# Performance work log

Measured on AMD Instinct MI355X. Metric: run time of the kernel, lower is better.

Reference implementation:

```python
import jax, jax.numpy as jnp
import numpy as np

B, T, D = 256, 512, 8      # batch, seq_len, Feature_number
H = 120                    # hidden_size
L = 4                      # layers=['s','s','s','s']
NH = D                     # num_heads = Feature_number
HD = H // NH               # head dim = 15
EPS = 1e-5


def setup_inputs() -> dict:
    key = jax.random.key(0)
    ks = jax.random.split(key, 16)
    rn = lambda k, shape, s=0.1: (jax.random.normal(k, shape, jnp.float32) * s)
    return {
        "x":   jax.random.normal(ks[0], (B, T, D), jnp.float32),
        # input->gate weights, stacked over layers
        "Wi":  rn(ks[1], (L, H, D)),
        "Wf":  rn(ks[2], (L, H, D)),
        "Wz":  rn(ks[3], (L, H, D)),
        "Wo":  rn(ks[4], (L, H, D)),
        # block-diagonal (multi-head) recurrent weights: [L, NH, HD, HD]
        "Ri":  rn(ks[5], (L, NH, HD, HD)),
        "Rf":  rn(ks[6], (L, NH, HD, HD)),
        "Rz":  rn(ks[7], (L, NH, HD, HD)),
        "Ro":  rn(ks[8], (L, NH, HD, HD)),
        "bi":  rn(ks[9],  (L, H), 0.02),
        "bf":  rn(ks[10], (L, H), 0.02),
        "bz":  rn(ks[11], (L, H), 0.02),
        "bo":  rn(ks[12], (L, H), 0.02),
        # per-block down-projection back to Feature_number (residual block)
        "Wp":  rn(ks[13], (L, D, H)),
        "bp":  jnp.zeros((L, D), jnp.float32),
        # BatchNorm1d(Feature_number) affine params
        "gamma": jnp.ones((D,), jnp.float32),
        "beta":  jnp.zeros((D,), jnp.float32),
        # fc5: Linear(Feature_number, 1)
        "Wfc": rn(ks[14], (1, D)),
        "bfc": jnp.zeros((1,), jnp.float32),
    }


def _slstm_layer(x, Wi, Wf, Wz, Wo, Ri, Rf, Rz, Ro, bi, bf, bz, bo, Wp, bp):
    """One sLSTM block: exp-gated recurrence with stabilizer, then down-proj + residual.
    x: [B, T, D] -> [B, T, D]."""
    Bn = x.shape[0]

    def rec(h, R):  # block-diagonal recurrent matmul: [B,H] x [NH,HD,HD] -> [B,H]
        return jnp.einsum("bnd,nde->bne", h.reshape(Bn, NH, HD), R).reshape(Bn, H)

    def step(carry, x_t):
        h, c, n, m = carry                       # each [B, H]
        it = x_t @ Wi.T + rec(h, Ri) + bi        # input gate pre-act
        ft = x_t @ Wf.T + rec(h, Rf) + bf        # forget gate pre-act (exp gating)
        z = jnp.tanh(x_t @ Wz.T + rec(h, Rz) + bz)
        o = jax.nn.sigmoid(x_t @ Wo.T + rec(h, Ro) + bo)
        m_new = jnp.maximum(ft + m, it)          # stabilizer state
        i_p = jnp.exp(it - m_new)
        f_p = jnp.exp(ft + m - m_new)
        c_new = f_p * c + i_p * z
        n_new = f_p * n + i_p                    # normalizer state
        h_new = o * (c_new / n_new)
        return (h_new, c_new, n_new, m_new), h_new

    z0 = jnp.zeros((Bn, H), x.dtype)
    (_, _, _, _), hs = jax.lax.scan(step, (z0, z0, z0, z0), jnp.swapaxes(x, 0, 1))
    y = jnp.einsum("tbh,dh->tbd", hs, Wp) + bp   # down-project to D
    return x + jnp.swapaxes(y, 0, 1)             # residual


def reference(x, Wi, Wf, Wz, Wo, Ri, Rf, Rz, Ro, bi, bf, bz, bo, Wp, bp,
              gamma, beta, Wfc, bfc):
    h = x
    for l in range(L):
        h = _slstm_layer(h, Wi[l], Wf[l], Wz[l], Wo[l], Ri[l], Rf[l], Rz[l], Ro[l],
                         bi[l], bf[l], bz[l], bo[l], Wp[l], bp[l])
    last = h[:, -1, :]                            # [B, D]
    # BatchNorm1d in training mode (batch stats, biased variance)
    mu = jnp.mean(last, axis=0)
    var = jnp.mean((last - mu) ** 2, axis=0)
    bn = (last - mu) / jnp.sqrt(var + EPS) * gamma + beta
    out = jax.nn.sigmoid(bn @ Wfc.T + bfc)        # [B, 1]
    return out[:, 0]                              # squeeze(1) -> [B]
```

## Files before the change

### kernel.cpp

```cpp
#include <hip/hip_runtime.h>
#include <math.h>

#define Bsz 256
#define T   512
#define Dd  8
#define Hh  120
#define Ll  4
#define NHn 8
#define HDd 15
#define HP  16
#define EPSf 1e-5f

__device__ __forceinline__ float fast_rcp(float x) {
#if __has_builtin(__builtin_amdgcn_rcpf)
    return __builtin_amdgcn_rcpf(x);
#else
    return 1.f / x;
#endif
}
__device__ __forceinline__ float tanh_fast(float x) {
    float e = __expf(2.f * x);
    return 1.f - 2.f * fast_rcp(e + 1.f);
}
__device__ __forceinline__ float sigm_fast(float x) {
    return fast_rcp(1.f + __expf(-x));
}

__global__ __launch_bounds__(512, 2) void slstm_kernel(
    const float* __restrict__ x,
    const float* __restrict__ Wi, const float* __restrict__ Wf,
    const float* __restrict__ Wz, const float* __restrict__ Wo,
    const float* __restrict__ Ri, const float* __restrict__ Rf,
    const float* __restrict__ Rz, const float* __restrict__ Ro,
    const float* __restrict__ bi, const float* __restrict__ bf,
    const float* __restrict__ bz, const float* __restrict__ bo,
    const float* __restrict__ Wp, const float* __restrict__ bp,
    float* __restrict__ last_out)
{
    __shared__ __align__(16) float xs[T * Dd];
    __shared__ __align__(16) float hb[Ll][2][NHn * HP];

    const int tid = threadIdx.x;
    const int b   = blockIdx.x;
    const int l   = tid >> 7;
    const int j   = tid & 127;

    {
        const float4* xg  = (const float4*)(x + (size_t)b * T * Dd);
        float4*       xs4 = (float4*)xs;
        xs4[tid]       = xg[tid];
        xs4[tid + 512] = xg[tid + 512];
        ((float*)hb)[tid]       = 0.f;
        ((float*)hb)[tid + 512] = 0.f;
    }

    const bool gl = (j < Hh);
    const int jj  = gl ? j : 0;
    const int n   = jj / HDd;
    const int e   = jj - n * HDd;
    float wI[Dd], wF[Dd], wZ[Dd], wO[Dd];
    float rI[HDd], rF[HDd], rZ[HDd], rO[HDd];
    {
        const int row = (l * Hh + jj) * Dd;
#pragma unroll
        for (int d = 0; d < Dd; ++d) {
            wI[d] = Wi[row + d]; wF[d] = Wf[row + d];
            wZ[d] = Wz[row + d]; wO[d] = Wo[row + d];
        }
        const int rb = ((l * NHn + n) * HDd) * HDd + e;
#pragma unroll
        for (int d = 0; d < HDd; ++d) {
            rI[d] = Ri[rb + d * HDd]; rF[d] = Rf[rb + d * HDd];
            rZ[d] = Rz[rb + d * HDd]; rO[d] = Ro[rb + d * HDd];
        }
    }
    float bI = bi[l * Hh + jj], bF = bf[l * Hh + jj];
    float bZ = bz[l * Hh + jj], bO = bo[l * Hh + jj];

    const int p  = (j >= 64) ? (j - 64) : j;
    const int d8 = p & 7, ch = p >> 3;
    float wp_r[16];
    {
        const int base = l * Dd * Hh + d8 * Hh + ch * HDd;
#pragma unroll
        for (int k = 0; k < HDd; ++k) wp_r[k] = Wp[base + k];
        wp_r[15] = 0.f;
    }
    float bp_r = bp[l * Dd + d8];

#pragma unroll
    for (int d = 0; d < Dd; ++d)
        asm volatile("" : "+v"(wI[d]), "+v"(wF[d]), "+v"(wZ[d]), "+v"(wO[d]));
#pragma unroll
    for (int d = 0; d < HDd; ++d)
        asm volatile("" : "+v"(rI[d]), "+v"(rF[d]), "+v"(rZ[d]), "+v"(rO[d]));
#pragma unroll
    for (int k = 0; k < 16; ++k)
        asm volatile("" : "+v"(wp_r[k]));
    asm volatile("" : "+v"(bI), "+v"(bF), "+v"(bZ), "+v"(bO));
    asm volatile("" : "+v"(bp_r));

    float cst = 0.f, nst = 0.f, mst = 0.f;

    __syncthreads();

    for (int tau = 0; tau < T + 2 * Ll - 1; ++tau) {
        const int t_g = tau - 2 * l;
        const int t_p = t_g - 1;

        if (gl && (t_g >= 0) && (t_g < T)) {
            const float4* xt4 = (const float4*)(xs + t_g * Dd);
            const float4 xa = xt4[0], xb2 = xt4[1];
            const float xv[Dd] = {xa.x, xa.y, xa.z, xa.w, xb2.x, xb2.y, xb2.z, xb2.w};
            float gi = bI, gf = bF, gz = bZ, go = bO;
#pragma unroll
            for (int d = 0; d < Dd; ++d) {
                gi = fmaf(xv[d], wI[d], gi);
                gf = fmaf(xv[d], wF[d], gf);
                gz = fmaf(xv[d], wZ[d], gz);
                go = fmaf(xv[d], wO[d], go);
            }
            const float4* h4 = (const float4*)(&hb[l][t_g & 1][n * HP]);
            const float4 h0 = h4[0], h1 = h4[1], h2 = h4[2], h3 = h4[3];
            const float hv[16] = {h0.x, h0.y, h0.z, h0.w, h1.x, h1.y, h1.z, h1.w,
                                  h2.x, h2.y, h2.z, h2.w, h3.x, h3.y, h3.z, h3.w};
#pragma unroll
            for (int d = 0; d < HDd; ++d) {
                gi = fmaf(hv[d], rI[d], gi);
                gf = fmaf(hv[d], rF[d], gf);
                gz = fmaf(hv[d], rZ[d], gz);
                go = fmaf(hv[d], rO[d], go);
            }
            const float z  = tanh_fast(gz);
            const float o  = sigm_fast(go);
            const float mn = fmaxf(gf + mst, gi);
            const float ip = __expf(gi - mn);
            const float fp = __expf(gf + mst - mn);
            cst = fmaf(fp, cst, ip * z);
            nst = fmaf(fp, nst, ip);
            mst = mn;
            const float hnew = o * cst * fast_rcp(nst);
            hb[l][(t_g & 1) ^ 1][n * HP + e] = hnew;
        }

        if ((j >= 64) && (t_p >= 0) && (t_p < T)) {
            const float4* h4 = (const float4*)(&hb[l][t_g & 1][ch * HP]);
            const float4 h0 = h4[0], h1 = h4[1], h2 = h4[2], h3 = h4[3];
            const float hv[16] = {h0.x, h0.y, h0.z, h0.w, h1.x, h1.y, h1.z, h1.w,
                                  h2.x, h2.y, h2.z, h2.w, h3.x, h3.y, h3.z, h3.w};
            float s = 0.f;
#pragma unroll
            for (int k = 0; k < 16; ++k) s = fmaf(hv[k], wp_r[k], s);
            s += __shfl_xor(s, 8);
            s += __shfl_xor(s, 16);
            s += __shfl_xor(s, 32);
            if (p < Dd) xs[t_p * Dd + p] += s + bp_r;
        }

        __syncthreads();
    }

    if (tid < Dd) last_out[b * Dd + tid] = xs[(T - 1) * Dd + tid];
}

__global__ __launch_bounds__(Bsz) void bn_fc_kernel(
    const float* __restrict__ last,
    const float* __restrict__ gamma, const float* __restrict__ beta,
    const float* __restrict__ Wfc,   const float* __restrict__ bfc,
    float* __restrict__ out)
{
    __shared__ float ls[Bsz][Dd];
    __shared__ float mu[Dd], rstdg[Dd], bet[Dd], wfc[Dd];
    const int tid = threadIdx.x;
#pragma unroll
    for (int d = 0; d < Dd; ++d) ls[tid][d] = last[tid * Dd + d];
    __syncthreads();
    if (tid < Dd) {
        float s = 0.f;
        for (int bb = 0; bb < Bsz; ++bb) s += ls[bb][tid];
        const float mean = s * (1.f / Bsz);
        float v = 0.f;
        for (int bb = 0; bb < Bsz; ++bb) {
            const float dd = ls[bb][tid] - mean;
            v += dd * dd;
        }
        v *= (1.f / Bsz);
        mu[tid]    = mean;
        rstdg[tid] = rsqrtf(v + EPSf) * gamma[tid];
        bet[tid]   = beta[tid];
        wfc[tid]   = Wfc[tid];
    }
    __syncthreads();
    float acc = bfc[0];
#pragma unroll
    for (int d = 0; d < Dd; ++d)
        acc += ((ls[tid][d] - mu[d]) * rstdg[d] + bet[d]) * wfc[d];
    out[tid] = sigm_fast(acc);
}

extern "C" void kernel_launch(void* const* d_in, const int* in_sizes, int n_in,
                              void* d_out, int out_size, void* d_ws, size_t ws_size,
                              hipStream_t stream) {
    const float* x    = (const float*)d_in[0];
    const float* Wi   = (const float*)d_in[1];
    const float* Wf   = (const float*)d_in[2];
    const float* Wz   = (const float*)d_in[3];
    const float* Wo   = (const float*)d_in[4];
    const float* Ri   = (const float*)d_in[5];
    const float* Rf   = (const float*)d_in[6];
    const float* Rz   = (const float*)d_in[7];
    const float* Ro   = (const float*)d_in[8];
    const float* bi   = (const float*)d_in[9];
    const float* bf   = (const float*)d_in[10];
    const float* bz   = (const float*)d_in[11];
    const float* bo   = (const float*)d_in[12];
    const float* Wp   = (const float*)d_in[13];
    const float* bp   = (const float*)d_in[14];
    const float* gamma= (const float*)d_in[15];
    const float* beta = (const float*)d_in[16];
    const float* Wfc  = (const float*)d_in[17];
    const float* bfc  = (const float*)d_in[18];

    float* last_ws = (float*)d_ws;
    float* out     = (float*)d_out;

    slstm_kernel<<<Bsz, 512, 0, stream>>>(x, Wi, Wf, Wz, Wo, Ri, Rf, Rz, Ro,
                                          bi, bf, bz, bo, Wp, bp, last_ws);
    bn_fc_kernel<<<1, Bsz, 0, stream>>>(last_ws, gamma, beta, Wfc, bfc, out);
}
```

Before: 453.1 us.

## Split each hidden unit's gates across two threads using packed FMAs

The block grows from 512 to 1024 threads. Each hidden unit is now handled by a thread pair: one lane computes the i/f pre-activations and the state update, the other computes z/o and passes them over with a lane shuffle. Each lane accumulates its two gates with 2-wide vector FMAs, which can map to packed FP32 instructions. The per-head stride in the shared hidden buffer is padded from 16 to 20 floats, likely to reduce LDS bank conflicts. This roughly halves the serial FMA chain per timestep, at the cost of extra shuffles, more resident threads and dropping the register-pinning asm.

After: 609.2 us. +34.4%, slower.

```diff
diff --git a/kernel.cpp b/kernel.cpp
--- a/kernel.cpp
+++ b/kernel.cpp
@@ -8,8 +8,10 @@
 #define Ll  4
 #define NHn 8
 #define HDd 15
-#define HP  16
+#define HP  20
 #define EPSf 1e-5f
+
+typedef float v2f __attribute__((ext_vector_type(2)));
 
 __device__ __forceinline__ float fast_rcp(float x) {
 #if __has_builtin(__builtin_amdgcn_rcpf)
@@ -25,8 +27,15 @@
 __device__ __forceinline__ float sigm_fast(float x) {
     return fast_rcp(1.f + __expf(-x));
 }
-
-__global__ __launch_bounds__(512, 2) void slstm_kernel(
+__device__ __forceinline__ v2f fma2(v2f a, v2f b, v2f c) {
+#if __has_builtin(__builtin_elementwise_fma)
+    return __builtin_elementwise_fma(a, b, c);
+#else
+    v2f r; r[0] = fmaf(a[0], b[0], c[0]); r[1] = fmaf(a[1], b[1], c[1]); return r;
+#endif
+}
+
+__global__ __launch_bounds__(1024, 4) void slstm_kernel(
     const float* __restrict__ x,
     const float* __restrict__ Wi, const float* __restrict__ Wf,
     const float* __restrict__ Wz, const float* __restrict__ Wo,
@@ -42,63 +51,49 @@
 
     const int tid = threadIdx.x;
     const int b   = blockIdx.x;
-    const int l   = tid >> 7;
-    const int j   = tid & 127;
+    const int l   = tid >> 8;
+    const int j   = tid & 255;
+    const int sub = j & 1;
+    const bool gl = (j < 2 * Hh);
+    const int u   = gl ? (j >> 1) : (Hh - 1);
+    const int n   = u / HDd;
+    const int e   = u - n * HDd;
 
     {
-        const float4* xg  = (const float4*)(x + (size_t)b * T * Dd);
-        float4*       xs4 = (float4*)xs;
-        xs4[tid]       = xg[tid];
-        xs4[tid + 512] = xg[tid + 512];
-        ((float*)hb)[tid]       = 0.f;
-        ((float*)hb)[tid + 512] = 0.f;
-    }
-
-    const bool gl = (j < Hh);
-    const int jj  = gl ? j : 0;
-    const int n   = jj / HDd;
-    const int e   = jj - n * HDd;
-    float wI[Dd], wF[Dd], wZ[Dd], wO[Dd];
-    float rI[HDd], rF[HDd], rZ[HDd], rO[HDd];
+        const float4* xg = (const float4*)(x + (size_t)b * T * Dd);
+        ((float4*)xs)[tid] = xg[tid];
+        float* hbf = (float*)hb;
+        hbf[tid < 1280 ? tid : 1279] = 0.f;
+        if (tid < 1280 - 1024) hbf[1024 + tid] = 0.f;
+    }
+
+    const float* Wa = sub ? Wz : Wi;
+    const float* Wb = sub ? Wo : Wf;
+    const float* Ra = sub ? Rz : Ri;
+    const float* Rb = sub ? Ro : Rf;
+    const float* ba = sub ? bz : bi;
+    const float* bb = sub ? bo : bf;
+
+    v2f w2[Dd], r2[HDd], bias2;
     {
-        const int row = (l * Hh + jj) * Dd;
-#pragma unroll
-        for (int d = 0; d < Dd; ++d) {
-            wI[d] = Wi[row + d]; wF[d] = Wf[row + d];
-            wZ[d] = Wz[row + d]; wO[d] = Wo[row + d];
-        }
+        const int row = (l * Hh + u) * Dd;
+#pragma unroll
+        for (int d = 0; d < Dd; ++d) { w2[d][0] = Wa[row + d]; w2[d][1] = Wb[row + d]; }
         const int rb = ((l * NHn + n) * HDd) * HDd + e;
 #pragma unroll
-        for (int d = 0; d < HDd; ++d) {
-            rI[d] = Ri[rb + d * HDd]; rF[d] = Rf[rb + d * HDd];
-            rZ[d] = Rz[rb + d * HDd]; rO[d] = Ro[rb + d * HDd];
-        }
-    }
-    float bI = bi[l * Hh + jj], bF = bf[l * Hh + jj];
-    float bZ = bz[l * Hh + jj], bO = bo[l * Hh + jj];
-
-    const int p  = (j >= 64) ? (j - 64) : j;
+        for (int k = 0; k < HDd; ++k) { r2[k][0] = Ra[rb + k * HDd]; r2[k][1] = Rb[rb + k * HDd]; }
+        bias2[0] = ba[l * Hh + u]; bias2[1] = bb[l * Hh + u];
+    }
+
+    const int p  = j & 63;
     const int d8 = p & 7, ch = p >> 3;
-    float wp_r[16];
+    float wp_r[HDd], bp_r;
     {
         const int base = l * Dd * Hh + d8 * Hh + ch * HDd;
 #pragma unroll
         for (int k = 0; k < HDd; ++k) wp_r[k] = Wp[base + k];
-        wp_r[15] = 0.f;
-    }
-    float bp_r = bp[l * Dd + d8];
-
-#pragma unroll
-    for (int d = 0; d < Dd; ++d)
-        asm volatile("" : "+v"(wI[d]), "+v"(wF[d]), "+v"(wZ[d]), "+v"(wO[d]));
-#pragma unroll
-    for (int d = 0; d < HDd; ++d)
-        asm volatile("" : "+v"(rI[d]), "+v"(rF[d]), "+v"(rZ[d]), "+v"(rO[d]));
-#pragma unroll
-    for (int k = 0; k < 16; ++k)
-        asm volatile("" : "+v"(wp_r[k]));
-    asm volatile("" : "+v"(bI), "+v"(bF), "+v"(bZ), "+v"(bO));
-    asm volatile("" : "+v"(bp_r));
+        bp_r = bp[l * Dd + d8];
+    }
 
     float cst = 0.f, nst = 0.f, mst = 0.f;
 
@@ -109,48 +104,44 @@
         const int t_p = t_g - 1;
 
         if (gl && (t_g >= 0) && (t_g < T)) {
+            const float* hcur = hb[l][t_g & 1];
             const float4* xt4 = (const float4*)(xs + t_g * Dd);
             const float4 xa = xt4[0], xb2 = xt4[1];
             const float xv[Dd] = {xa.x, xa.y, xa.z, xa.w, xb2.x, xb2.y, xb2.z, xb2.w};
-            float gi = bI, gf = bF, gz = bZ, go = bO;
-#pragma unroll
-            for (int d = 0; d < Dd; ++d) {
-                gi = fmaf(xv[d], wI[d], gi);
-                gf = fmaf(xv[d], wF[d], gf);
-                gz = fmaf(xv[d], wZ[d], gz);
-                go = fmaf(xv[d], wO[d], go);
-            }
-            const float4* h4 = (const float4*)(&hb[l][t_g & 1][n * HP]);
+            const float4* h4 = (const float4*)(hcur + n * HP);
             const float4 h0 = h4[0], h1 = h4[1], h2 = h4[2], h3 = h4[3];
             const float hv[16] = {h0.x, h0.y, h0.z, h0.w, h1.x, h1.y, h1.z, h1.w,
                                   h2.x, h2.y, h2.z, h2.w, h3.x, h3.y, h3.z, h3.w};
-#pragma unroll
-            for (int d = 0; d < HDd; ++d) {
-                gi = fmaf(hv[d], rI[d], gi);
-                gf = fmaf(hv[d], rF[d], gf);
-                gz = fmaf(hv[d], rZ[d], gz);
-                go = fmaf(hv[d], rO[d], go);
+            v2f g2 = bias2;
+#pragma unroll
+            for (int d = 0; d < Dd; ++d)  g2 = fma2((v2f){xv[d], xv[d]}, w2[d], g2);
+#pragma unroll
+            for (int k = 0; k < HDd; ++k) g2 = fma2((v2f){hv[k], hv[k]}, r2[k], g2);
+
+            float zv = 0.f, ov = 0.f;
+            if (sub) { zv = tanh_fast(g2[0]); ov = sigm_fast(g2[1]); }
+            const float zr = __shfl_xor(zv, 1);
+            const float orr = __shfl_xor(ov, 1);
+            if (!sub) {
+                const float it = g2[0], ft = g2[1];
+                const float mn = fmaxf(ft + mst, it);
+                const float ip = __expf(it - mn);
+                const float fp = __expf(ft + mst - mn);
+                cst = fmaf(fp, cst, ip * zr);
+                nst = fmaf(fp, nst, ip);
+                mst = mn;
+                hb[l][(t_g & 1) ^ 1][n * HP + e] = orr * cst * fast_rcp(nst);
             }
-            const float z  = tanh_fast(gz);
-            const float o  = sigm_fast(go);
-            const float mn = fmaxf(gf + mst, gi);
-            const float ip = __expf(gi - mn);
-            const float fp = __expf(gf + mst - mn);
-            cst = fmaf(fp, cst, ip * z);
-            nst = fmaf(fp, nst, ip);
-            mst = mn;
-            const float hnew = o * cst * fast_rcp(nst);
-            hb[l][(t_g & 1) ^ 1][n * HP + e] = hnew;
         }
 
-        if ((j >= 64) && (t_p >= 0) && (t_p < T)) {
-            const float4* h4 = (const float4*)(&hb[l][t_g & 1][ch * HP]);
+        if ((j < 64) && (t_p >= 0) && (t_p < T)) {
+            const float4* h4 = (const float4*)(hb[l][t_g & 1] + ch * HP);
             const float4 h0 = h4[0], h1 = h4[1], h2 = h4[2], h3 = h4[3];
             const float hv[16] = {h0.x, h0.y, h0.z, h0.w, h1.x, h1.y, h1.z, h1.w,
                                   h2.x, h2.y, h2.z, h2.w, h3.x, h3.y, h3.z, h3.w};
             float s = 0.f;
 #pragma unroll
-            for (int k = 0; k < 16; ++k) s = fmaf(hv[k], wp_r[k], s);
+            for (int k = 0; k < HDd; ++k) s = fmaf(hv[k], wp_r[k], s);
             s += __shfl_xor(s, 8);
             s += __shfl_xor(s, 16);
             s += __shfl_xor(s, 32);
@@ -224,7 +215,7 @@
     float* last_ws = (float*)d_ws;
     float* out     = (float*)d_out;
 
-    slstm_kernel<<<Bsz, 512, 0, stream>>>(x, Wi, Wf, Wz, Wo, Ri, Rf, Rz, Ro,
-                                          bi, bf, bz, bo, Wp, bp, last_ws);
+    slstm_kernel<<<Bsz, 1024, 0, stream>>>(x, Wi, Wf, Wz, Wo, Ri, Rf, Rz, Ro,
+                                           bi, bf, bz, bo, Wp, bp, last_ws);
     bn_fc_kernel<<<1, Bsz, 0, stream>>>(last_ws, gamma, beta, Wfc, bfc, out);
 }
```
